# Performance work log

Hardware: AMD Instinct MI355X
Metric: run time of the kernel (lower is better)

## Reference

```python
import jax, jax.numpy as jnp
import numpy as np

N = 50000
E = 1600000
IN_C = 128
HID = 64
HEADS = 4
OUT_C = 64
NEG_SLOPE = 0.2


def gat_layer(x, src, dst, W, a_src, a_dst, b, heads, ch):
    # x: [N, F_in], W: [F_in, heads*ch], a_src/a_dst: [heads, ch], b: [heads*ch]
    n = x.shape[0]
    h = (x @ W).reshape(n, heads, ch)                       # [N, H, C]
    alpha_s = jnp.einsum('nhc,hc->nh', h, a_src)            # [N, H]
    alpha_d = jnp.einsum('nhc,hc->nh', h, a_dst)
    e = jax.nn.leaky_relu(alpha_s[src] + alpha_d[dst], NEG_SLOPE)  # [Et, H]
    # segment softmax over incoming edges of each dst node (self-loops guarantee non-empty)
    m = jax.ops.segment_max(e, dst, num_segments=n)
    ex = jnp.exp(e - m[dst])
    denom = jax.ops.segment_sum(ex, dst, num_segments=n)
    alpha = ex / (denom[dst] + 1e-16)                       # [Et, H]
    out = jax.ops.segment_sum(h[src] * alpha[:, :, None], dst, num_segments=n)  # [N,H,C]
    return out.reshape(n, heads * ch) + b


def setup_inputs() -> dict:
    key = jax.random.key(0)
    ks = jax.random.split(key, 10)
    x = jax.random.normal(ks[0], (N, IN_C), dtype=jnp.float32)
    edge_index = jax.random.randint(ks[1], (2, E), 0, N, dtype=jnp.int64)
    s = 0.1
    W1 = jax.random.normal(ks[2], (IN_C, HEADS * HID), dtype=jnp.float32) * s
    a_src1 = jax.random.normal(ks[3], (HEADS, HID), dtype=jnp.float32) * s
    a_dst1 = jax.random.normal(ks[4], (HEADS, HID), dtype=jnp.float32) * s
    b1 = jnp.zeros((HEADS * HID,), dtype=jnp.float32)
    W2 = jax.random.normal(ks[5], (HEADS * HID, OUT_C), dtype=jnp.float32) * s
    a_src2 = jax.random.normal(ks[6], (1, OUT_C), dtype=jnp.float32) * s
    a_dst2 = jax.random.normal(ks[7], (1, OUT_C), dtype=jnp.float32) * s
    b2 = jnp.zeros((OUT_C,), dtype=jnp.float32)
    return {"x": x, "edge_index": edge_index, "W1": W1, "a_src1": a_src1,
            "a_dst1": a_dst1, "b1": b1, "W2": W2, "a_src2": a_src2,
            "a_dst2": a_dst2, "b2": b2}


def reference(x, edge_index, W1, a_src1, a_dst1, b1, W2, a_src2, a_dst2, b2):
    # add self-loops (PyG GATConv default)
    loops = jnp.arange(N, dtype=edge_index.dtype)
    src = jnp.concatenate([edge_index[0], loops])
    dst = jnp.concatenate([edge_index[1], loops])
    h = gat_layer(x, src, dst, W1, a_src1, a_dst1, b1, HEADS, HID)
    h = jax.nn.relu(h)
    out = gat_layer(h, src, dst, W2, a_src2, a_dst2, b2, 1, OUT_C)
    return out
```

## Files before the change

kernel.cpp:

```cpp
#include <hip/hip_runtime.h>
#include <cstdint>
#include <cstddef>

#define IN_C 128
#define CAP 72
#define PCAP 36

typedef _Float16 __attribute__((ext_vector_type(2))) half2v;
typedef _Float16 __attribute__((ext_vector_type(4))) half4v;
typedef _Float16 __attribute__((ext_vector_type(8))) f16x8;
typedef float    __attribute__((ext_vector_type(4))) f32x4;
typedef unsigned __attribute__((ext_vector_type(2))) u32x2;
typedef unsigned __attribute__((ext_vector_type(4))) u32x4;

static __device__ __forceinline__ float lrelu(float x) { return x > 0.f ? x : 0.2f * x; }

static __device__ __forceinline__ unsigned pack2h(float a, float b) {
  union { _Float16 h[2]; unsigned u; } c;
  c.h[0] = (_Float16)a; c.h[1] = (_Float16)b;
  return c.u;
}
static __device__ __forceinline__ half2v bc_h2(unsigned u) {
  union { unsigned u; half2v h; } c; c.u = u; return c.h;
}

#if __has_builtin(__builtin_amdgcn_fdot2)
static __device__ __forceinline__ float FDOT2(half2v a, half2v b, float c) {
  return __builtin_amdgcn_fdot2(a, b, c, false);
}
#else
static __device__ __forceinline__ float FDOT2(half2v a, half2v b, float c) {
  return c + (float)a.x * (float)b.x + (float)a.y * (float)b.y;
}
#endif

__global__ void k_scatter_cnt(const int* __restrict__ ei_src, const int* __restrict__ ei_dst,
                              int* __restrict__ cnt, int* __restrict__ s32,
                              int E, int Et, int nPerReg, int n) {
  int r = blockIdx.x & 7;
  int base = (blockIdx.x >> 3) * 1024 + threadIdx.x;
  int lo = r * nPerReg;
  int hi = lo + nPerReg; if (hi > n) hi = n;
#pragma unroll
  for (int k = 0; k < 4; ++k) {
    int e = base + k * 256;
    if (e >= Et) continue;
    int d = (e < E) ? __builtin_nontemporal_load(&ei_dst[e]) : (e - E);
    if (d < lo || d >= hi) continue;
    int s = (e < E) ? __builtin_nontemporal_load(&ei_src[e]) : d;
    int pos = atomicAdd(&cnt[d], 1);
    if (pos < CAP) s32[(size_t)d * CAP + pos] = s;
  }
}

__global__ void k_edgew(const int* __restrict__ s32, const int* __restrict__ cnt,
                        const float* __restrict__ as1, const float* __restrict__ ad1,
                        u32x2* __restrict__ spair, u32x4* __restrict__ wpair, int ptotal) {
  int i = blockIdx.x * 256 + threadIdx.x;
  if (i >= ptotal) return;
  int node = (int)((unsigned)i / PCAP);
  int p = i - node * PCAP;
  int c = cnt[node]; if (c > CAP) c = CAP;
  int npair = (c + 1) >> 1;
  if (p >= npair) return;
  int s0 = s32[(size_t)node * CAP + 2 * p];
  bool has1 = (2 * p + 1) < c;
  int s1 = has1 ? s32[(size_t)node * CAP + 2 * p + 1] : s0;
  float4 bd = *(const float4*)&ad1[(size_t)node * 4];
  float4 a0 = *(const float4*)&as1[(size_t)s0 * 4];
  float4 a1 = *(const float4*)&as1[(size_t)s1 * 4];
  float A0 = __expf(lrelu(a0.x + bd.x)), A1 = __expf(lrelu(a0.y + bd.y));
  float A2 = __expf(lrelu(a0.z + bd.z)), A3 = __expf(lrelu(a0.w + bd.w));
  float B0 = 0.f, B1 = 0.f, B2 = 0.f, B3 = 0.f;
  if (has1) {
    B0 = __expf(lrelu(a1.x + bd.x)); B1 = __expf(lrelu(a1.y + bd.y));
    B2 = __expf(lrelu(a1.z + bd.z)); B3 = __expf(lrelu(a1.w + bd.w));
  }
  u32x4 wp = {pack2h(A0, B0), pack2h(A1, B1), pack2h(A2, B2), pack2h(A3, B3)};
  u32x2 sp = {(unsigned)s0, (unsigned)s1};
  wpair[i] = wp;
  spair[i] = sp;
}

__global__ void k_edgew2(const int* __restrict__ s32, const int* __restrict__ cnt,
                         const float* __restrict__ as2, const float* __restrict__ ad2,
                         u32x2* __restrict__ sw2, int total) {
  int i = blockIdx.x * 256 + threadIdx.x;
  if (i >= total) return;
  int node = (int)((unsigned)i / CAP);
  int slot = i - node * CAP;
  int c = cnt[node]; if (c > CAP) c = CAP;
  if (slot >= c) return;
  int s = s32[i];
  float w = __expf(lrelu(as2[s] + ad2[node]));
  union { float f; unsigned u; } cv; cv.f = w;
  u32x2 o = {(unsigned)s, cv.u};
  sw2[i] = o;
}

__global__ void k_prep(const float* __restrict__ x, const float* __restrict__ W1,
                       const float* __restrict__ W2, const float* __restrict__ as_,
                       const float* __restrict__ ad_, _Float16* __restrict__ xh,
                       _Float16* __restrict__ W1t, _Float16* __restrict__ W2t,
                       float* __restrict__ V, int n4, int xb, int wb) {
  int b = blockIdx.x;
  if (b < xb) {
    int i = b * 256 + threadIdx.x;
    if (i >= n4) return;
    f32x4 v = __builtin_nontemporal_load((const f32x4*)&x[i * 4]);
    half4v o;
    o.x = (_Float16)v.x; o.y = (_Float16)v.y; o.z = (_Float16)v.z; o.w = (_Float16)v.w;
    *(half4v*)&xh[i * 4] = o;
  } else if (b < xb + wb) {
    int i = (b - xb) * 256 + threadIdx.x;
    if (i < 128 * 256) {
      int k = i / 256, nn = i % 256;
      W1t[(size_t)nn * 128 + k] = (_Float16)W1[i];
    } else {
      int j = i - 128 * 256;
      if (j < 256 * 64) {
        int k = j / 64, nn = j % 64;
        W2t[(size_t)nn * 256 + k] = (_Float16)W2[j];
      }
    }
  } else {
    int t = (b - xb - wb) * 256 + threadIdx.x;
    if (t >= 1024) return;
    int h = t >> 7, k = t & 127;
    int hh = h & 3;
    const float* av = (h < 4) ? as_ : ad_;
    float s = 0.f;
#pragma unroll 8
    for (int c = 0; c < 64; ++c) s += W1[k * 256 + hh * 64 + c] * av[hh * 64 + c];
    V[h * 128 + k] = s;
  }
}

__launch_bounds__(256)
__global__ void k_alpha1x(const _Float16* __restrict__ xh, const float* __restrict__ V,
                          float* __restrict__ as1, float* __restrict__ ad1, int n) {
  __shared__ float Vs[1024];
  int tid = threadIdx.x;
  for (int i = tid; i < 1024; i += 256) Vs[i] = V[i];
  __syncthreads();
  int wave = tid >> 6, lane = tid & 63;
  int node = blockIdx.x * 4 + wave;
  if (node >= n) return;
  half2v hv = *(const half2v*)&xh[(size_t)node * 128 + lane * 2];
  float x0 = (float)hv.x, x1 = (float)hv.y;
  float r[8];
#pragma unroll
  for (int h = 0; h < 8; ++h)
    r[h] = x0 * Vs[h * 128 + lane * 2] + x1 * Vs[h * 128 + lane * 2 + 1];
#pragma unroll
  for (int off = 1; off < 64; off <<= 1) {
#pragma unroll
    for (int h = 0; h < 8; ++h) r[h] += __shfl_xor(r[h], off);
  }
  if (lane == 0) {
#pragma unroll
    for (int h = 0; h < 4; ++h) {
      as1[node * 4 + h] = r[h];
      ad1[node * 4 + h] = r[4 + h];
    }
  }
}

__launch_bounds__(256)
__global__ void k_aggr1x(const int* __restrict__ cnt, const u32x2* __restrict__ spair,
                         const u32x4* __restrict__ wpair, const _Float16* __restrict__ xh,
                         _Float16* __restrict__ agg, int n) {
  int wave = threadIdx.x >> 6, lane = threadIdx.x & 63;
  int node = blockIdx.x * 4 + wave;
  if (node >= n) return;
  int deg = cnt[node]; if (deg > CAP) deg = CAP;
  int npair = (deg + 1) >> 1;
  int base = node * PCAP;
  int g = lane >> 5, l32 = lane & 31;
  int ch0 = l32 * 4;
  const half2v ONE2 = bc_h2(0x3C003C00u);
  float acc[4][4] = {};
  float ds[4] = {};
  for (int p0 = 0; p0 < npair; p0 += 4) {
    int pA = base + p0 + g;
    int pB = pA + 2;
    int lim = base + npair;
    unsigned s0 = 0, s1 = 0, s2 = 0, s3 = 0;
    u32x4 wA = {0, 0, 0, 0}, wB = {0, 0, 0, 0};
    if (pA < lim) { u32x2 sp = spair[pA]; s0 = sp.x; s1 = sp.y; wA = wpair[pA]; }
    if (pB < lim) { u32x2 sp = spair[pB]; s2 = sp.x; s3 = sp.y; wB = wpair[pB]; }
    u32x2 xa = *(const u32x2*)&xh[(size_t)s0 * 128 + ch0];
    u32x2 xb = *(const u32x2*)&xh[(size_t)s1 * 128 + ch0];
    u32x2 xc = *(const u32x2*)&xh[(size_t)s2 * 128 + ch0];
    u32x2 xd = *(const u32x2*)&xh[(size_t)s3 * 128 + ch0];
    {
      half2v P0 = bc_h2(wA.x), P1 = bc_h2(wA.y), P2 = bc_h2(wA.z), P3 = bc_h2(wA.w);
      half2v Q0 = bc_h2((xa.x & 0xffffu) | (xb.x << 16));
      half2v Q1 = bc_h2((xa.x >> 16) | (xb.x & 0xffff0000u));
      half2v Q2 = bc_h2((xa.y & 0xffffu) | (xb.y << 16));
      half2v Q3 = bc_h2((xa.y >> 16) | (xb.y & 0xffff0000u));
      ds[0] = FDOT2(P0, ONE2, ds[0]); ds[1] = FDOT2(P1, ONE2, ds[1]);
      ds[2] = FDOT2(P2, ONE2, ds[2]); ds[3] = FDOT2(P3, ONE2, ds[3]);
      acc[0][0] = FDOT2(P0, Q0, acc[0][0]); acc[0][1] = FDOT2(P0, Q1, acc[0][1]);
      acc[0][2] = FDOT2(P0, Q2, acc[0][2]); acc[0][3] = FDOT2(P0, Q3, acc[0][3]);
      acc[1][0] = FDOT2(P1, Q0, acc[1][0]); acc[1][1] = FDOT2(P1, Q1, acc[1][1]);
      acc[1][2] = FDOT2(P1, Q2, acc[1][2]); acc[1][3] = FDOT2(P1, Q3, acc[1][3]);
      acc[2][0] = FDOT2(P2, Q0, acc[2][0]); acc[2][1] = FDOT2(P2, Q1, acc[2][1]);
      acc[2][2] = FDOT2(P2, Q2, acc[2][2]); acc[2][3] = FDOT2(P2, Q3, acc[2][3]);
      acc[3][0] = FDOT2(P3, Q0, acc[3][0]); acc[3][1] = FDOT2(P3, Q1, acc[3][1]);
      acc[3][2] = FDOT2(P3, Q2, acc[3][2]); acc[3][3] = FDOT2(P3, Q3, acc[3][3]);
    }
    {
      half2v P0 = bc_h2(wB.x), P1 = bc_h2(wB.y), P2 = bc_h2(wB.z), P3 = bc_h2(wB.w);
      half2v Q0 = bc_h2((xc.x & 0xffffu) | (xd.x << 16));
      half2v Q1 = bc_h2((xc.x >> 16) | (xd.x & 0xffff0000u));
      half2v Q2 = bc_h2((xc.y & 0xffffu) | (xd.y << 16));
      half2v Q3 = bc_h2((xc.y >> 16) | (xd.y & 0xffff0000u));
      ds[0] = FDOT2(P0, ONE2, ds[0]); ds[1] = FDOT2(P1, ONE2, ds[1]);
      ds[2] = FDOT2(P2, ONE2, ds[2]); ds[3] = FDOT2(P3, ONE2, ds[3]);
      acc[0][0] = FDOT2(P0, Q0, acc[0][0]); acc[0][1] = FDOT2(P0, Q1, acc[0][1]);
      acc[0][2] = FDOT2(P0, Q2, acc[0][2]); acc[0][3] = FDOT2(P0, Q3, acc[0][3]);
      acc[1][0] = FDOT2(P1, Q0, acc[1][0]); acc[1][1] = FDOT2(P1, Q1, acc[1][1]);
      acc[1][2] = FDOT2(P1, Q2, acc[1][2]); acc[1][3] = FDOT2(P1, Q3, acc[1][3]);
      acc[2][0] = FDOT2(P2, Q0, acc[2][0]); acc[2][1] = FDOT2(P2, Q1, acc[2][1]);
      acc[2][2] = FDOT2(P2, Q2, acc[2][2]); acc[2][3] = FDOT2(P2, Q3, acc[2][3]);
      acc[3][0] = FDOT2(P3, Q0, acc[3][0]); acc[3][1] = FDOT2(P3, Q1, acc[3][1]);
      acc[3][2] = FDOT2(P3, Q2, acc[3][2]); acc[3][3] = FDOT2(P3, Q3, acc[3][3]);
    }
  }
#pragma unroll
  for (int h = 0; h < 4; ++h) {
    ds[h] += __shfl_xor(ds[h], 32);
#pragma unroll
    for (int j = 0; j < 4; ++j) acc[h][j] += __shfl_xor(acc[h][j], 32);
  }
  if (g == 0) {
#pragma unroll
    for (int h = 0; h < 4; ++h) {
      float inv = 1.0f / (ds[h] + 1e-16f);
      half4v o;
      o.x = (_Float16)(acc[h][0] * inv);
      o.y = (_Float16)(acc[h][1] * inv);
      o.z = (_Float16)(acc[h][2] * inv);
      o.w = (_Float16)(acc[h][3] * inv);
      *(half4v*)&agg[(size_t)node * 512 + h * 128 + ch0] = o;
    }
  }
}

__launch_bounds__(256)
__global__ void k_gemm1b(const _Float16* __restrict__ agg, const _Float16* __restrict__ W1t,
                         const float* __restrict__ b1, _Float16* __restrict__ hrelu, int M) {
  int w = threadIdx.x >> 6, lane = threadIdx.x & 63;
  int r = lane & 15, kg = lane >> 4;
  int m0 = blockIdx.x * 64 + w * 16;
  f32x4 acc[16];
#pragma unroll
  for (int c = 0; c < 16; ++c) acc[c] = (f32x4){0.f, 0.f, 0.f, 0.f};
  int mA = m0 + r; if (mA > M - 1) mA = M - 1;
  const _Float16* Arow = agg + (size_t)mA * 512 + kg * 8;
#pragma unroll
  for (int k0 = 0; k0 < 128; k0 += 32) {
    f16x8 a[4];
#pragma unroll
    for (int h = 0; h < 4; ++h) a[h] = *(const f16x8*)(Arow + h * 128 + k0);
#pragma unroll
    for (int c = 0; c < 16; ++c) {
      f16x8 b = *(const f16x8*)&W1t[(size_t)(c * 16 + r) * 128 + k0 + kg * 8];
      acc[c] = __builtin_amdgcn_mfma_f32_16x16x32_f16(a[c >> 2], b, acc[c], 0, 0, 0);
    }
  }
#pragma unroll
  for (int c = 0; c < 16; ++c) {
    float bv = b1[c * 16 + r];
#pragma unroll
    for (int j = 0; j < 4; ++j) {
      int m = m0 + kg * 4 + j;
      if (m < M) hrelu[(size_t)m * 256 + c * 16 + r] = (_Float16)fmaxf(acc[c][j] + bv, 0.f);
    }
  }
}

__launch_bounds__(256)
__global__ void k_gemm2_a(const _Float16* __restrict__ A, const _Float16* __restrict__ Bt,
                          const float* __restrict__ a_s, const float* __restrict__ a_d,
                          _Float16* __restrict__ C, float* __restrict__ as2,
                          float* __restrict__ ad2, int M) {
  int w = threadIdx.x >> 6, lane = threadIdx.x & 63;
  int r = lane & 15, kg = lane >> 4;
  int m0 = blockIdx.x * 64 + w * 16;
  f32x4 acc[4];
#pragma unroll
  for (int c = 0; c < 4; ++c) acc[c] = (f32x4){0.f, 0.f, 0.f, 0.f};
  int mA = m0 + r; if (mA > M - 1) mA = M - 1;
  const _Float16* Arow = A + (size_t)mA * 256 + kg * 8;
#pragma unroll
  for (int k0 = 0; k0 < 256; k0 += 32) {
    f16x8 a = *(const f16x8*)(Arow + k0);
#pragma unroll
    for (int c = 0; c < 4; ++c) {
      f16x8 b = *(const f16x8*)&Bt[(size_t)(c * 16 + r) * 256 + k0 + kg * 8];
      acc[c] = __builtin_amdgcn_mfma_f32_16x16x32_f16(a, b, acc[c], 0, 0, 0);
    }
  }
  float sp[4] = {}, dp[4] = {};
#pragma unroll
  for (int c = 0; c < 4; ++c) {
    float asv = a_s[c * 16 + r];
    float adv = a_d[c * 16 + r];
#pragma unroll
    for (int j = 0; j < 4; ++j) {
      float v = acc[c][j];
      sp[j] += v * asv;
      dp[j] += v * adv;
    }
  }
#pragma unroll
  for (int off = 1; off < 16; off <<= 1) {
#pragma unroll
    for (int j = 0; j < 4; ++j) {
      sp[j] += __shfl_xor(sp[j], off);
      dp[j] += __shfl_xor(dp[j], off);
    }
  }
#pragma unroll
  for (int c = 0; c < 4; ++c) {
#pragma unroll
    for (int j = 0; j < 4; ++j) {
      int m = m0 + kg * 4 + j;
      if (m < M) C[(size_t)m * 64 + c * 16 + r] = (_Float16)acc[c][j];
    }
  }
  if (r == 0) {
#pragma unroll
    for (int j = 0; j < 4; ++j) {
      int m = m0 + kg * 4 + j;
      if (m < M) { as2[m] = sp[j]; ad2[m] = dp[j]; }
    }
  }
}

__launch_bounds__(256)
__global__ void k_aggr2(const int* __restrict__ cnt, const u32x2* __restrict__ sw2,
                        const _Float16* __restrict__ h2h, const float* __restrict__ b2,
                        float* __restrict__ out, int n) {
  int wave = threadIdx.x >> 6, lane = threadIdx.x & 63;
  int node = blockIdx.x * 4 + wave;
  if (node >= n) return;
  int deg = cnt[node]; if (deg > CAP) deg = CAP;
  int beg = node * CAP, end = beg + deg;
  int g = lane >> 4, l16 = lane & 15;
  int ch0 = l16 * 4;
  float acc[4] = {};
  float dsum = 0.f;
  for (int i = beg; i < end; i += 4) {
    int idx = i + g;
    int s = 0; float w = 0.f;
    if (idx < end) {
      u32x2 r = sw2[idx];
      s = (int)r.x;
      union { unsigned u; float f; } c; c.u = r.y; w = c.f;
    }
    half4v hv = *(const half4v*)&h2h[(size_t)s * 64 + ch0];
    dsum += w;
    acc[0] += w * (float)hv.x; acc[1] += w * (float)hv.y;
    acc[2] += w * (float)hv.z; acc[3] += w * (float)hv.w;
  }
#pragma unroll
  for (int off = 16; off < 64; off <<= 1) {
    dsum += __shfl_xor(dsum, off);
#pragma unroll
    for (int j = 0; j < 4; ++j) acc[j] += __shfl_xor(acc[j], off);
  }
  if (g == 0) {
    float inv = 1.0f / (dsum + 1e-16f);
    float4 o;
    o.x = acc[0] * inv + b2[ch0];
    o.y = acc[1] * inv + b2[ch0 + 1];
    o.z = acc[2] * inv + b2[ch0 + 2];
    o.w = acc[3] * inv + b2[ch0 + 3];
    *(float4*)&out[(size_t)node * 64 + ch0] = o;
  }
}

extern "C" void kernel_launch(void* const* d_in, const int* in_sizes, int n_in,
                              void* d_out, int out_size, void* d_ws, size_t ws_size,
                              hipStream_t stream) {
  const float* x    = (const float*)d_in[0];
  const int*   ei   = (const int*)d_in[1];
  const float* W1   = (const float*)d_in[2];
  const float* a_s1 = (const float*)d_in[3];
  const float* a_d1 = (const float*)d_in[4];
  const float* b1   = (const float*)d_in[5];
  const float* W2   = (const float*)d_in[6];
  const float* a_s2 = (const float*)d_in[7];
  const float* a_d2 = (const float*)d_in[8];
  const float* b2   = (const float*)d_in[9];
  float* out = (float*)d_out;

  const int n  = in_sizes[0] / IN_C;
  const int E  = in_sizes[1] / 2;
  const int Et = E + n;
  const int* ei_src = ei;
  const int* ei_dst = ei + E;

  char* ws = (char*)d_ws;
  size_t off = 0;
  auto alloc = [&](size_t bytes) -> void* {
    void* p = ws + off;
    off = (off + bytes + 255) & ~(size_t)255;
    return p;
  };
  _Float16* xh      = (_Float16*)alloc((size_t)n * 128 * 2);
  _Float16* W1t     = (_Float16*)alloc((size_t)256 * 128 * 2);
  _Float16* W2t     = (_Float16*)alloc((size_t)64 * 256 * 2);
  float*    V       = (float*)alloc((size_t)1024 * 4);
  _Float16* agg     = (_Float16*)alloc((size_t)n * 512 * 2);
  _Float16* hrelu_h = (_Float16*)alloc((size_t)n * 256 * 2);
  _Float16* h2h     = (_Float16*)alloc((size_t)n * 64 * 2);
  float* as1        = (float*)alloc((size_t)n * 4 * 4);
  float* ad1        = (float*)alloc((size_t)n * 4 * 4);
  float* as2        = (float*)alloc((size_t)n * 4);
  float* ad2        = (float*)alloc((size_t)n * 4);
  int* cnt          = (int*)alloc((size_t)n * 4);
  int* s32          = (int*)alloc((size_t)n * CAP * 4);
  u32x2* spair      = (u32x2*)alloc((size_t)n * PCAP * 8);
  u32x4* wpair      = (u32x4*)alloc((size_t)n * PCAP * 16);
  u32x2* sw2        = (u32x2*)alloc((size_t)n * CAP * 8);

  int nw  = (n + 3) / 4;
  int gx1 = (n + 63) / 64;
  int nPerReg = (n + 7) / 8;
  int n4  = n * 128 / 4;
  int xb  = (n4 + 255) / 256;
  int wb  = (128 * 256 + 256 * 64 + 255) / 256;
  int sb  = (Et + 1023) / 1024;
  int total  = n * CAP;
  int ptotal = n * PCAP;
  int tb  = (total + 255) / 256;
  int pb  = (ptotal + 255) / 256;

  (void)hipMemsetAsync(cnt, 0, (size_t)n * 4, stream);
  hipLaunchKernelGGL(k_scatter_cnt, dim3(sb * 8), dim3(256), 0, stream,
                     ei_src, ei_dst, cnt, s32, E, Et, nPerReg, n);

  hipLaunchKernelGGL(k_prep, dim3(xb + wb + 4), dim3(256), 0, stream,
                     x, W1, W2, a_s1, a_d1, xh, W1t, W2t, V, n4, xb, wb);
  hipLaunchKernelGGL(k_alpha1x, dim3(nw), dim3(256), 0, stream, xh, V, as1, ad1, n);

  hipLaunchKernelGGL(k_edgew, dim3(pb), dim3(256), 0, stream, s32, cnt, as1, ad1, spair, wpair, ptotal);
  hipLaunchKernelGGL(k_aggr1x, dim3(nw), dim3(256), 0, stream, cnt, spair, wpair, xh, agg, n);
  hipLaunchKernelGGL(k_gemm1b, dim3(gx1), dim3(256), 0, stream, agg, W1t, b1, hrelu_h, n);

  hipLaunchKernelGGL(k_gemm2_a, dim3(gx1), dim3(256), 0, stream,
                     hrelu_h, W2t, a_s2, a_d2, h2h, as2, ad2, n);
  hipLaunchKernelGGL(k_edgew2, dim3(tb), dim3(256), 0, stream, s32, cnt, as2, ad2, sw2, total);
  hipLaunchKernelGGL(k_aggr2, dim3(nw), dim3(256), 0, stream, cnt, sw2, h2h, b2, out, n);
}
```

Measured before the change: 352.5 us.

## Pre-bucket edges by destination region before CSR scatter

Replaces the 8x-redundant scatter, where every block re-read all edges and kept only its region, with two passes. The first pass reads edges once and partitions (src,dst) pairs into 8 region buckets, using wave ballots plus shared and global atomics. The second pass scatters each bucket into the per-node slot lists, with block indices interleaved across regions to keep atomic locality. The aim is to remove the repeated edge-array reads, at the cost of an extra memset, an intermediate buffer write and read, and a fixed bucket capacity that could overflow on skewed graphs.

```diff
diff --git a/kernel.cpp b/kernel.cpp
--- a/kernel.cpp
+++ b/kernel.cpp
@@ -5,6 +5,7 @@
 #define IN_C 128
 #define CAP 72
 #define PCAP 36
+#define BSTRIDE 16
 
 typedef _Float16 __attribute__((ext_vector_type(2))) half2v;
 typedef _Float16 __attribute__((ext_vector_type(4))) half4v;
@@ -34,22 +35,68 @@
 }
 #endif
 
-__global__ void k_scatter_cnt(const int* __restrict__ ei_src, const int* __restrict__ ei_dst,
-                              int* __restrict__ cnt, int* __restrict__ s32,
-                              int E, int Et, int nPerReg, int n) {
-  int r = blockIdx.x & 7;
-  int base = (blockIdx.x >> 3) * 1024 + threadIdx.x;
-  int lo = r * nPerReg;
-  int hi = lo + nPerReg; if (hi > n) hi = n;
+__global__ void k_bucket(const int* __restrict__ ei_src, const int* __restrict__ ei_dst,
+                         int* __restrict__ bcnt, u32x2* __restrict__ bucket,
+                         int E, int Et, int nPerReg, int bcap) {
+  __shared__ int lcnt[8], lbase[8];
+  int tid = threadIdx.x;
+  int lane = tid & 63;
+  if (tid < 8) lcnt[tid] = 0;
+  __syncthreads();
+  int base = blockIdx.x * 1024 + tid;
+  int rr[4], off[4], ss[4], dd[4];
 #pragma unroll
   for (int k = 0; k < 4; ++k) {
     int e = base + k * 256;
-    if (e >= Et) continue;
-    int d = (e < E) ? __builtin_nontemporal_load(&ei_dst[e]) : (e - E);
-    if (d < lo || d >= hi) continue;
-    int s = (e < E) ? __builtin_nontemporal_load(&ei_src[e]) : d;
-    int pos = atomicAdd(&cnt[d], 1);
-    if (pos < CAP) s32[(size_t)d * CAP + pos] = s;
+    bool act = e < Et;
+    int d = 0, s = 0;
+    if (act) {
+      d = (e < E) ? __builtin_nontemporal_load(&ei_dst[e]) : (e - E);
+      s = (e < E) ? __builtin_nontemporal_load(&ei_src[e]) : d;
+    }
+    int r = act ? (int)((unsigned)d / (unsigned)nPerReg) : -1;
+    if (r > 7) r = 7;
+    rr[k] = r; ss[k] = s; dd[k] = d; off[k] = 0;
+#pragma unroll
+    for (int q = 0; q < 8; ++q) {
+      unsigned long long m = __ballot(r == q);
+      if (m == 0) continue;
+      int lead = (int)(__ffsll((long long)m) - 1);
+      unsigned long long below = lane ? (m & (~0ull >> (64 - lane))) : 0ull;
+      int rank = (int)__popcll(below);
+      int wbase = 0;
+      if (lane == lead) wbase = atomicAdd(&lcnt[q], (int)__popcll(m));
+      wbase = __shfl(wbase, lead);
+      if (r == q) off[k] = wbase + rank;
+    }
+  }
+  __syncthreads();
+  if (tid < 8) lbase[tid] = atomicAdd(&bcnt[tid * BSTRIDE], lcnt[tid]);
+  __syncthreads();
+#pragma unroll
+  for (int k = 0; k < 4; ++k) {
+    int r = rr[k];
+    if (r < 0) continue;
+    int pos = lbase[r] + off[k];
+    if (pos < bcap) {
+      u32x2 rec = {(unsigned)ss[k], (unsigned)dd[k]};
+      bucket[(size_t)r * bcap + pos] = rec;
+    }
+  }
+}
+
+__global__ void k_scatter2(const u32x2* __restrict__ bucket, const int* __restrict__ bcnt,
+                           int* __restrict__ cnt, int* __restrict__ s32, int bcap) {
+  int r = blockIdx.x & 7;
+  int m = bcnt[r * BSTRIDE]; if (m > bcap) m = bcap;
+  int base = (blockIdx.x >> 3) * 1024 + threadIdx.x;
+#pragma unroll
+  for (int k = 0; k < 4; ++k) {
+    int i = base + k * 256;
+    if (i >= m) continue;
+    u32x2 p = bucket[(size_t)r * bcap + i];
+    int pos = atomicAdd(&cnt[p.y], 1);
+    if (pos < CAP) s32[(size_t)p.y * CAP + pos] = (int)p.x;
   }
 }
 
@@ -427,6 +474,9 @@
   u32x2* spair      = (u32x2*)alloc((size_t)n * PCAP * 8);
   u32x4* wpair      = (u32x4*)alloc((size_t)n * PCAP * 16);
   u32x2* sw2        = (u32x2*)alloc((size_t)n * CAP * 8);
+  int* bcnt         = (int*)alloc((size_t)8 * BSTRIDE * 4);
+  int bcap          = ((Et / 8 + 16384 + 1023) / 1024) * 1024;
+  u32x2* bucket     = (u32x2*)alloc((size_t)8 * bcap * 8);
 
   int nw  = (n + 3) / 4;
   int gx1 = (n + 63) / 64;
@@ -439,10 +489,14 @@
   int ptotal = n * PCAP;
   int tb  = (total + 255) / 256;
   int pb  = (ptotal + 255) / 256;
+  int s2b = (bcap + 1023) / 1024;
 
   (void)hipMemsetAsync(cnt, 0, (size_t)n * 4, stream);
-  hipLaunchKernelGGL(k_scatter_cnt, dim3(sb * 8), dim3(256), 0, stream,
-                     ei_src, ei_dst, cnt, s32, E, Et, nPerReg, n);
+  (void)hipMemsetAsync(bcnt, 0, (size_t)8 * BSTRIDE * 4, stream);
+  hipLaunchKernelGGL(k_bucket, dim3(sb), dim3(256), 0, stream,
+                     ei_src, ei_dst, bcnt, bucket, E, Et, nPerReg, bcap);
+  hipLaunchKernelGGL(k_scatter2, dim3(s2b * 8), dim3(256), 0, stream,
+                     bucket, bcnt, cnt, s32, bcap);
 
   hipLaunchKernelGGL(k_prep, dim3(xb + wb + 4), dim3(256), 0, stream,
                      x, W1, W2, a_s1, a_d1, xh, W1t, W2t, V, n4, xb, wb);
```

Result: slower. 386.5 us (+9.6%).
